# Kernel tuning notes

Hardware: AMD Instinct MI355X
Metric: run time of the kernel (lower is better)

The kernel has to match this reference:

```python
import jax, jax.numpy as jnp
import numpy as np

N, K, E = 262144, 8, 16
DT = 0.02  # config.delta_time


def _mono(x, w1, b1, w2, b2):
    # monotonic_fun with increasing=False: out_linear(exp(-in_linear(x)))
    return jnp.exp(-(x @ w1.T + b1)) @ w2.T + b2


def _isin(a, b):
    # rowwise torch.isin: a [N,P], b [N,Q] -> [N,P] bool
    return (a[:, :, None] == b[:, None, :]).any(-1)


def _angle_clamp(vec, v, ang):
    # torch.cosine_similarity(v, vec, dim=-1).abs() > ang gate (eps=1e-8)
    num = jnp.einsum('nd,nrd->nr', v, vec)
    den = jnp.maximum(jnp.linalg.norm(v, axis=-1)[:, None] * jnp.linalg.norm(vec, axis=-1), 1e-8)
    keep = jnp.abs(num / den) > ang
    return jnp.where(keep[..., None], vec, 0.0)


def _linear_params(key, fan_in, fan_out):
    a = 1.0 / np.sqrt(fan_in)
    k1, k2 = jax.random.split(key)
    # weightConstraint(min_b=0) clamps weights to >= 0 at init
    w = jnp.maximum(jax.random.uniform(k1, (fan_out, fan_in), minval=-a, maxval=a), 0.0)
    b = jax.random.uniform(k2, (fan_out,), minval=-a, maxval=a)
    return w, b


def _mono_params(key):
    k1, k2 = jax.random.split(key)
    w1, b1 = _linear_params(k1, 1, E)
    w2, b2 = _linear_params(k2, E, 1)
    return w1, b1, w2, b2


def setup_inputs() -> dict:
    key = jax.random.key(0)
    ks = jax.random.split(key, 12)
    ego = jax.random.normal(ks[0], (N, 16), dtype=jnp.float32)
    ego = ego.at[:, 0].set(jnp.arange(N, dtype=jnp.float32))
    # surrounding-vehicle id columns 7..14 as small integer ids (floats)
    ego = ego.at[:, 7:15].set(jax.random.randint(ks[1], (N, 8), 0, 21).astype(jnp.float32))
    nei = jax.random.normal(ks[2], (N, K, 16), dtype=jnp.float32)
    nei = nei.at[:, :, 0].set(jax.random.randint(ks[3], (N, K), 1, 21).astype(jnp.float32))
    border = jax.random.uniform(ks[4], (4,), dtype=jnp.float32) * 10.0 + 1.0
    recording_time = jnp.zeros((N, K, 2), dtype=jnp.float32)
    p_dest = jax.random.uniform(ks[5], (2,), dtype=jnp.float32)  # relu(rand(2))
    angle = jax.nn.sigmoid(jax.random.uniform(ks[6], (1,), dtype=jnp.float32))
    d = {'ego': ego, 'nei': nei, 'border': border, 'recording_time': recording_time,
         'p_dest': p_dest, 'angle': angle}
    for name, kk in (('rep', ks[7]), ('att', ks[8]), ('bor', ks[9]), ('del', ks[10])):
        w1, b1, w2, b2 = _mono_params(kk)
        d[name + '_w1'], d[name + '_b1'], d[name + '_w2'], d[name + '_b2'] = w1, b1, w2, b2
    return d


def reference(ego, nei, border, recording_time, p_dest, angle,
              rep_w1, rep_b1, rep_w2, rep_b2,
              att_w1, att_b1, att_w2, att_b2,
              bor_w1, bor_b1, bor_w2, bor_b2,
              del_w1, del_b1, del_w2, del_b2):
    ang = angle[0]
    v = ego[:, 3:5]                                        # ego velocity [N,2]
    speed = jnp.linalg.norm(v, axis=-1)
    desired = jnp.stack([speed, jnp.zeros_like(speed)], axis=1)
    f_dest = ((p_dest[1] * desired - v) / p_dest[0])[:, None, :]   # [N,1,2]

    nei_id = nei[:, :, 0]                                  # [N,K]
    idx = _isin(nei_id, ego[:, 7:15]) & (nei_id != 0)

    # --- recording_time buffer update (vectorized remain/new/pad concat) ---
    buf_id, buf_ct = recording_time[:, :, 0], recording_time[:, :, 1]
    ifin = _isin(buf_id, nei_id)                           # buffer slots still present
    ct2 = buf_ct + ifin.astype(buf_ct.dtype)               # increment their counts
    ifnew = (~_isin(nei_id, buf_id)) & (nei_id != 0)       # brand-new neighbor ids
    cand = jnp.concatenate([jnp.stack([buf_id, ct2], -1),
                            jnp.stack([nei_id, jnp.ones_like(nei_id)], -1)], axis=1)  # [N,2K,2]
    ar = jnp.arange(K)
    BIG = 1 << 20
    keyord = jnp.concatenate([jnp.where(ifin, ar, BIG), jnp.where(ifnew, ar + K, BIG)], axis=1)
    order = jnp.argsort(keyord, axis=1)[:, :K]             # stable: remain order, then new, then pad
    skey = jnp.take_along_axis(keyord, order, axis=1)
    new_buf = jnp.where((skey < BIG)[..., None],
                        jnp.take_along_axis(cand, order[..., None], axis=1), 1.0)  # pad with ones
    count = new_buf[:, :, 1]                               # [N,K]

    # --- neighbor attraction / repulsion ---
    r = jnp.where(idx[..., None], nei[:, :, 1:3] - ego[:, None, 1:3], 0.0)
    rn = jnp.linalg.norm(r, axis=-1)
    rns = jnp.where(idx, rn, 1.0)                          # safe divisor (masked slots zeroed below)
    dirn = r / rns[..., None]
    f_attr = (_mono(count[..., None], del_w1, del_b1, del_w2, del_b2)
              * _mono(rn[..., None], att_w1, att_b1, att_w2, att_b2) * dirn)
    v_nei = nei[:, :, 3:5]
    b = rn + jnp.sum((r + v_nei * DT) ** 2, -1) - jnp.sum((v_nei * DT) ** 2, -1)
    b = jnp.sqrt(jnp.maximum(jnp.where(idx, b, 1.0), 1e-12)) / 2.0
    f_repu = _mono(b[..., None], rep_w1, rep_b1, rep_w2, rep_b2) * dirn
    f_attr = jnp.where(idx[..., None], f_attr, 0.0)
    f_repu = jnp.where(idx[..., None], f_repu, 0.0)

    # --- border repulsion (y-axis only), select_lane = [0, -1] ---
    rb_all = ego[:, 2:3] - border                          # [N,4]
    rb = jnp.stack([rb_all[:, 0], rb_all[:, -1]], axis=1)  # [N,2]
    rbn = jnp.abs(rb)
    f_by = _mono(rbn[..., None], bor_w1, bor_b1, bor_w2, bor_b2) * (rb / rbn)[..., None]
    f_bor = jnp.concatenate([jnp.zeros_like(f_by), f_by], axis=-1)  # [N,2,2]

    f_destination = _angle_clamp(f_dest, v, ang).sum(1)
    f_neighbors = _angle_clamp(f_attr, v, ang).sum(1) + _angle_clamp(f_repu, v, ang).sum(1)
    f_border = _angle_clamp(f_bor, v, ang).sum(1)
    return jnp.stack([f_destination, f_neighbors, f_border], axis=1)  # [N,3,2]
```

## Files before the change

### kernel.cpp

```cpp
#include <hip/hip_runtime.h>
#include <math.h>

#define EN 16

__device__ __forceinline__ float mono_fast(float x,
    const float* __restrict__ w1, const float* __restrict__ b1,
    const float* __restrict__ w2, const float* __restrict__ b2) {
    float acc = 0.0f;
#pragma unroll
    for (int e = 0; e < EN; ++e) {
        float pre = fmaf(x, w1[e], b1[e]);
        acc = fmaf(__expf(-pre), w2[e], acc);
    }
    return acc + b2[0];
}

extern "C" __global__ void __launch_bounds__(256)
sfm_kernel(const float* __restrict__ ego, const float* __restrict__ nei,
           const float* __restrict__ border, const float* __restrict__ rec,
           const float* __restrict__ p_dest, const float* __restrict__ angle,
           const float* __restrict__ rep_w1, const float* __restrict__ rep_b1,
           const float* __restrict__ rep_w2, const float* __restrict__ rep_b2,
           const float* __restrict__ att_w1, const float* __restrict__ att_b1,
           const float* __restrict__ att_w2, const float* __restrict__ att_b2,
           const float* __restrict__ bor_w1, const float* __restrict__ bor_b1,
           const float* __restrict__ bor_w2, const float* __restrict__ bor_b2,
           const float* __restrict__ del_w1, const float* __restrict__ del_b1,
           const float* __restrict__ del_w2, const float* __restrict__ del_b2,
           float* __restrict__ out, int N)
{
    const int gid = blockIdx.x * blockDim.x + threadIdx.x;
    const int n = gid >> 3;
    const int k = gid & 7;
    if (n >= N) return;
    const int lane = threadIdx.x & 63;
    const int gbase = lane & ~7;

    const float ang = angle[0];
    const float p0 = p_dest[0], p1 = p_dest[1];

    const float* er = ego + (size_t)n * 16;
    float4 ea = *(const float4*)(er);
    float4 eb = *(const float4*)(er + 4);
    float4 ec = *(const float4*)(er + 8);
    float4 ed = *(const float4*)(er + 12);
    const float px = ea.y, py = ea.z, vx = ea.w, vy = eb.x;
    const float speed = sqrtf(vx * vx + vy * vy);

    const float* nb = nei + (size_t)n * 128 + (size_t)k * 16;
    float4 na = *(const float4*)nb;
    const float nvyv = nb[4];
    const float nid = na.x;

    float2 rc = *(const float2*)(rec + (size_t)n * 16 + (size_t)k * 2);
    const float bid = rc.x, bct = rc.y;

    bool fin = (bid == nid);
#pragma unroll
    for (int t = 1; t < 8; ++t)
        fin = fin || (bid == __shfl_xor(nid, t));

    unsigned long long bal = __ballot(fin);
    unsigned finM = (unsigned)((bal >> gbase) & 0xFFull);
    int popcFin = __popc(finM);
    int jsel = 0, cbits = 0;
#pragma unroll
    for (int j = 0; j < 8; ++j) {
        int bit = (finM >> j) & 1;
        if (bit && cbits == k) jsel = j;
        cbits += bit;
    }
    float bctj = __shfl(bct, gbase + jsel);
    float cntk = (k < popcFin) ? (bctj + 1.0f) : 1.0f;

    bool match = (nid == eb.w) || (nid == ec.x) || (nid == ec.y) || (nid == ec.z)
              || (nid == ec.w) || (nid == ed.x) || (nid == ed.y) || (nid == ed.z);
    const bool idxk = match && (nid != 0.0f);

    float rx = idxk ? (na.y - px) : 0.0f;
    float ry = idxk ? (na.z - py) : 0.0f;
    float rn = sqrtf(rx * rx + ry * ry);
    float rns = idxk ? rn : 1.0f;
    float dx = rx / rns, dy = ry / rns;

    float att = mono_fast(rn,   att_w1, att_b1, att_w2, att_b2);
    float del = mono_fast(cntk, del_w1, del_b1, del_w2, del_b2);
    float sa = del * att;
    float fax = idxk ? sa * dx : 0.0f;
    float fay = idxk ? sa * dy : 0.0f;

    float nbx = 0.0f, nby = 0.0f;
    {
        float num = vx * fax + vy * fay;
        float fn = sqrtf(fax * fax + fay * fay);
        float den = fmaxf(speed * fn, 1e-8f);
        if (fabsf(num / den) > ang) { nbx += fax; nby += fay; }
    }

    float sxv = na.w * 0.02f, syv = nvyv * 0.02f;
    float ox = rx + sxv, oy = ry + syv;
    float bsum = rn + (ox * ox + oy * oy) - (sxv * sxv + syv * syv);
    float bgate = idxk ? bsum : 1.0f;
    float bb = sqrtf(fmaxf(bgate, 1e-12f)) * 0.5f;
    float rep = mono_fast(bb, rep_w1, rep_b1, rep_w2, rep_b2);
    float frx = idxk ? rep * dx : 0.0f;
    float fry = idxk ? rep * dy : 0.0f;
    {
        float num = vx * frx + vy * fry;
        float fn = sqrtf(frx * frx + fry * fry);
        float den = fmaxf(speed * fn, 1e-8f);
        if (fabsf(num / den) > ang) { nbx += frx; nby += fry; }
    }

    float bsel = (k == 0) ? border[0] : border[3];
    float rb = py - bsel;
    float rbn = fabsf(rb);
    float mb = mono_fast(rbn, bor_w1, bor_b1, bor_w2, bor_b2);
    float fby = mb * (rb / rbn);
    float bory = 0.0f;
    {
        float num = vy * fby;
        float den = fmaxf(speed * fabsf(fby), 1e-8f);
        if ((fabsf(num / den) > ang) && (k < 2)) bory = fby;
    }

#pragma unroll
    for (int m = 1; m < 8; m <<= 1) {
        nbx  += __shfl_xor(nbx,  m);
        nby  += __shfl_xor(nby,  m);
        bory += __shfl_xor(bory, m);
    }

    float fdx = (p1 * speed - vx) / p0;
    float fdy = (0.0f - vy) / p0;
    float fdex = 0.0f, fdey = 0.0f;
    {
        float num = vx * fdx + vy * fdy;
        float fn = sqrtf(fdx * fdx + fdy * fdy);
        float den = fmaxf(speed * fn, 1e-8f);
        if (fabsf(num / den) > ang) { fdex = fdx; fdey = fdy; }
    }

    float wv = (k == 0) ? fdex
             : (k == 1) ? fdey
             : (k == 2) ? nbx
             : (k == 3) ? nby
             : (k == 4) ? 0.0f
             : bory;
    if (k < 6) out[(size_t)n * 6 + k] = wv;
}

extern "C" void kernel_launch(void* const* d_in, const int* in_sizes, int n_in,
                              void* d_out, int out_size, void* d_ws, size_t ws_size,
                              hipStream_t stream) {
    const float* ego    = (const float*)d_in[0];
    const float* nei    = (const float*)d_in[1];
    const float* border = (const float*)d_in[2];
    const float* rec    = (const float*)d_in[3];
    const float* p_dest = (const float*)d_in[4];
    const float* angle  = (const float*)d_in[5];
    const float* rep_w1 = (const float*)d_in[6];
    const float* rep_b1 = (const float*)d_in[7];
    const float* rep_w2 = (const float*)d_in[8];
    const float* rep_b2 = (const float*)d_in[9];
    const float* att_w1 = (const float*)d_in[10];
    const float* att_b1 = (const float*)d_in[11];
    const float* att_w2 = (const float*)d_in[12];
    const float* att_b2 = (const float*)d_in[13];
    const float* bor_w1 = (const float*)d_in[14];
    const float* bor_b1 = (const float*)d_in[15];
    const float* bor_w2 = (const float*)d_in[16];
    const float* bor_b2 = (const float*)d_in[17];
    const float* del_w1 = (const float*)d_in[18];
    const float* del_b1 = (const float*)d_in[19];
    const float* del_w2 = (const float*)d_in[20];
    const float* del_b2 = (const float*)d_in[21];
    float* out = (float*)d_out;

    int N = in_sizes[0] / 16;
    long long threads = (long long)N * 8;
    dim3 grid((unsigned)((threads + 255) / 256));
    sfm_kernel<<<grid, 256, 0, stream>>>(
        ego, nei, border, rec, p_dest, angle,
        rep_w1, rep_b1, rep_w2, rep_b2,
        att_w1, att_b1, att_w2, att_b2,
        bor_w1, bor_b1, bor_w2, bor_b2,
        del_w1, del_b1, del_w2, del_b2,
        out, N);
}
```

Measured before the change: 255.3 us.

## Process all eight neighbors per thread instead of one thread per neighbor

Remaps the kernel from eight lanes per agent to one thread per agent, looping over the eight neighbors in registers. This removes the cross-lane shuffles and ballot, the redundant per-lane ego and destination work, and the six unused border-repulsion evaluations per agent. In exchange, each thread holds many more live registers, which may lower occupancy. Per-thread strided loads of 512-byte neighbor rows may also coalesce worse than the previous layout.

```diff
diff --git a/kernel.cpp b/kernel.cpp
--- a/kernel.cpp
+++ b/kernel.cpp
@@ -29,12 +29,8 @@
            const float* __restrict__ del_w2, const float* __restrict__ del_b2,
            float* __restrict__ out, int N)
 {
-    const int gid = blockIdx.x * blockDim.x + threadIdx.x;
-    const int n = gid >> 3;
-    const int k = gid & 7;
+    const int n = blockIdx.x * blockDim.x + threadIdx.x;
     if (n >= N) return;
-    const int lane = threadIdx.x & 63;
-    const int gbase = lane & ~7;
 
     const float ang = angle[0];
     const float p0 = p_dest[0], p1 = p_dest[1];
@@ -47,88 +43,122 @@
     const float px = ea.y, py = ea.z, vx = ea.w, vy = eb.x;
     const float speed = sqrtf(vx * vx + vy * vy);
 
-    const float* nb = nei + (size_t)n * 128 + (size_t)k * 16;
-    float4 na = *(const float4*)nb;
-    const float nvyv = nb[4];
-    const float nid = na.x;
-
-    float2 rc = *(const float2*)(rec + (size_t)n * 16 + (size_t)k * 2);
-    const float bid = rc.x, bct = rc.y;
-
-    bool fin = (bid == nid);
-#pragma unroll
-    for (int t = 1; t < 8; ++t)
-        fin = fin || (bid == __shfl_xor(nid, t));
-
-    unsigned long long bal = __ballot(fin);
-    unsigned finM = (unsigned)((bal >> gbase) & 0xFFull);
-    int popcFin = __popc(finM);
-    int jsel = 0, cbits = 0;
-#pragma unroll
-    for (int j = 0; j < 8; ++j) {
-        int bit = (finM >> j) & 1;
-        if (bit && cbits == k) jsel = j;
-        cbits += bit;
-    }
-    float bctj = __shfl(bct, gbase + jsel);
-    float cntk = (k < popcFin) ? (bctj + 1.0f) : 1.0f;
-
-    bool match = (nid == eb.w) || (nid == ec.x) || (nid == ec.y) || (nid == ec.z)
-              || (nid == ec.w) || (nid == ed.x) || (nid == ed.y) || (nid == ed.z);
-    const bool idxk = match && (nid != 0.0f);
-
-    float rx = idxk ? (na.y - px) : 0.0f;
-    float ry = idxk ? (na.z - py) : 0.0f;
-    float rn = sqrtf(rx * rx + ry * ry);
-    float rns = idxk ? rn : 1.0f;
-    float dx = rx / rns, dy = ry / rns;
-
-    float att = mono_fast(rn,   att_w1, att_b1, att_w2, att_b2);
-    float del = mono_fast(cntk, del_w1, del_b1, del_w2, del_b2);
-    float sa = del * att;
-    float fax = idxk ? sa * dx : 0.0f;
-    float fay = idxk ? sa * dy : 0.0f;
-
-    float nbx = 0.0f, nby = 0.0f;
+    const float* nb = nei + (size_t)n * 128;
+    float4 na[8]; float nvy[8];
+#pragma unroll
+    for (int k = 0; k < 8; ++k) {
+        na[k]  = *(const float4*)(nb + k * 16);
+        nvy[k] = nb[k * 16 + 4];
+    }
+
+    const float* rr = rec + (size_t)n * 16;
+    float bid[8], bct[8];
+#pragma unroll
+    for (int q = 0; q < 4; ++q) {
+        float4 t = *(const float4*)(rr + q * 4);
+        bid[2*q]   = t.x; bct[2*q]   = t.y;
+        bid[2*q+1] = t.z; bct[2*q+1] = t.w;
+    }
+
+    unsigned finM = 0;
+#pragma unroll
+    for (int k = 0; k < 8; ++k) {
+        bool fin = false;
+#pragma unroll
+        for (int j = 0; j < 8; ++j) fin = fin || (bid[k] == na[j].x);
+        finM |= (fin ? 1u : 0u) << k;
+    }
+    const int popcFin = __popc(finM);
+
+    float cnt[8];
+#pragma unroll
+    for (int k = 0; k < 8; ++k) {
+        int jsel = 0, cbits = 0;
+#pragma unroll
+        for (int j = 0; j < 8; ++j) {
+            int bit = (finM >> j) & 1;
+            if (bit && cbits == k) jsel = j;
+            cbits += bit;
+        }
+        float bj = bct[0];
+#pragma unroll
+        for (int j = 1; j < 8; ++j) bj = (jsel == j) ? bct[j] : bj;
+        cnt[k] = (k < popcFin) ? (bj + 1.0f) : 1.0f;
+    }
+
+    float sx[4] = {0.f, 0.f, 0.f, 0.f}, sy[4] = {0.f, 0.f, 0.f, 0.f};
+#pragma unroll
+    for (int k = 0; k < 8; ++k) {
+        const float nid = na[k].x;
+        bool match = (nid == eb.w) || (nid == ec.x) || (nid == ec.y) || (nid == ec.z)
+                  || (nid == ec.w) || (nid == ed.x) || (nid == ed.y) || (nid == ed.z);
+        const bool idxk = match && (nid != 0.0f);
+
+        float rx = idxk ? (na[k].y - px) : 0.0f;
+        float ry = idxk ? (na[k].z - py) : 0.0f;
+        float rn = sqrtf(rx * rx + ry * ry);
+        float rns = idxk ? rn : 1.0f;
+        float dx = rx / rns, dy = ry / rns;
+
+        float att = mono_fast(rn,     att_w1, att_b1, att_w2, att_b2);
+        float del = mono_fast(cnt[k], del_w1, del_b1, del_w2, del_b2);
+        float sa = del * att;
+        float fax = idxk ? sa * dx : 0.0f;
+        float fay = idxk ? sa * dy : 0.0f;
+
+        float cxk = 0.0f, cyk = 0.0f;
+        {
+            float num = vx * fax + vy * fay;
+            float fn = sqrtf(fax * fax + fay * fay);
+            float den = fmaxf(speed * fn, 1e-8f);
+            if (fabsf(num / den) > ang) { cxk += fax; cyk += fay; }
+        }
+
+        float sxv = na[k].w * 0.02f, syv = nvy[k] * 0.02f;
+        float ox = rx + sxv, oy = ry + syv;
+        float bsum = rn + (ox * ox + oy * oy) - (sxv * sxv + syv * syv);
+        float bgate = idxk ? bsum : 1.0f;
+        float bb = sqrtf(fmaxf(bgate, 1e-12f)) * 0.5f;
+        float rep = mono_fast(bb, rep_w1, rep_b1, rep_w2, rep_b2);
+        float frx = idxk ? rep * dx : 0.0f;
+        float fry = idxk ? rep * dy : 0.0f;
+        {
+            float num = vx * frx + vy * fry;
+            float fn = sqrtf(frx * frx + fry * fry);
+            float den = fmaxf(speed * fn, 1e-8f);
+            if (fabsf(num / den) > ang) { cxk += frx; cyk += fry; }
+        }
+
+        sx[k >> 1] += cxk;
+        sy[k >> 1] += cyk;
+    }
+    const float nbx = (sx[0] + sx[1]) + (sx[2] + sx[3]);
+    const float nby = (sy[0] + sy[1]) + (sy[2] + sy[3]);
+
+    float bory;
     {
-        float num = vx * fax + vy * fay;
-        float fn = sqrtf(fax * fax + fay * fay);
-        float den = fmaxf(speed * fn, 1e-8f);
-        if (fabsf(num / den) > ang) { nbx += fax; nby += fay; }
-    }
-
-    float sxv = na.w * 0.02f, syv = nvyv * 0.02f;
-    float ox = rx + sxv, oy = ry + syv;
-    float bsum = rn + (ox * ox + oy * oy) - (sxv * sxv + syv * syv);
-    float bgate = idxk ? bsum : 1.0f;
-    float bb = sqrtf(fmaxf(bgate, 1e-12f)) * 0.5f;
-    float rep = mono_fast(bb, rep_w1, rep_b1, rep_w2, rep_b2);
-    float frx = idxk ? rep * dx : 0.0f;
-    float fry = idxk ? rep * dy : 0.0f;
-    {
-        float num = vx * frx + vy * fry;
-        float fn = sqrtf(frx * frx + fry * fry);
-        float den = fmaxf(speed * fn, 1e-8f);
-        if (fabsf(num / den) > ang) { nbx += frx; nby += fry; }
-    }
-
-    float bsel = (k == 0) ? border[0] : border[3];
-    float rb = py - bsel;
-    float rbn = fabsf(rb);
-    float mb = mono_fast(rbn, bor_w1, bor_b1, bor_w2, bor_b2);
-    float fby = mb * (rb / rbn);
-    float bory = 0.0f;
-    {
-        float num = vy * fby;
-        float den = fmaxf(speed * fabsf(fby), 1e-8f);
-        if ((fabsf(num / den) > ang) && (k < 2)) bory = fby;
-    }
-
-#pragma unroll
-    for (int m = 1; m < 8; m <<= 1) {
-        nbx  += __shfl_xor(nbx,  m);
-        nby  += __shfl_xor(nby,  m);
-        bory += __shfl_xor(bory, m);
+        float b0v = border[0], b3v = border[3];
+
+        float rb0 = py - b0v, rbn0 = fabsf(rb0);
+        float mb0 = mono_fast(rbn0, bor_w1, bor_b1, bor_w2, bor_b2);
+        float fby0 = mb0 * (rb0 / rbn0);
+        float g0 = 0.0f;
+        {
+            float num = vy * fby0;
+            float den = fmaxf(speed * fabsf(fby0), 1e-8f);
+            if (fabsf(num / den) > ang) g0 = fby0;
+        }
+
+        float rb1 = py - b3v, rbn1 = fabsf(rb1);
+        float mb1 = mono_fast(rbn1, bor_w1, bor_b1, bor_w2, bor_b2);
+        float fby1 = mb1 * (rb1 / rbn1);
+        float g1 = 0.0f;
+        {
+            float num = vy * fby1;
+            float den = fmaxf(speed * fabsf(fby1), 1e-8f);
+            if (fabsf(num / den) > ang) g1 = fby1;
+        }
+        bory = g0 + g1;
     }
 
     float fdx = (p1 * speed - vx) / p0;
@@ -141,13 +171,10 @@
         if (fabsf(num / den) > ang) { fdex = fdx; fdey = fdy; }
     }
 
-    float wv = (k == 0) ? fdex
-             : (k == 1) ? fdey
-             : (k == 2) ? nbx
-             : (k == 3) ? nby
-             : (k == 4) ? 0.0f
-             : bory;
-    if (k < 6) out[(size_t)n * 6 + k] = wv;
+    float2* o = (float2*)(out + (size_t)n * 6);
+    o[0] = make_float2(fdex, fdey);
+    o[1] = make_float2(nbx, nby);
+    o[2] = make_float2(0.0f, bory);
 }
 
 extern "C" void kernel_launch(void* const* d_in, const int* in_sizes, int n_in,
@@ -178,8 +205,7 @@
     float* out = (float*)d_out;
 
     int N = in_sizes[0] / 16;
-    long long threads = (long long)N * 8;
-    dim3 grid((unsigned)((threads + 255) / 256));
+    dim3 grid((unsigned)((N + 255) / 256));
     sfm_kernel<<<grid, 256, 0, stream>>>(
         ego, nei, border, rec, p_dest, angle,
         rep_w1, rep_b1, rep_w2, rep_b2,
```

After: 272.5 us. 1.07x slower.

## Process two neighbors per thread with four lanes per agent

Applied to the files above, without the earlier changes.

Remaps the kernel so each agent uses four lanes instead of eight, with each lane handling two neighbors. The recording-time lookup is rebuilt from two ballots and interleaved bitmasks, and outputs are written as float2. This halves the redundant per-lane ego loads, border evaluations, destination math and shuffle-reduction steps. The cost is more registers and serial work per thread, and less thread-level parallelism for hiding memory latency.

```diff
diff --git a/kernel.cpp b/kernel.cpp
--- a/kernel.cpp
+++ b/kernel.cpp
@@ -13,6 +13,60 @@
         acc = fmaf(__expf(-pre), w2[e], acc);
     }
     return acc + b2[0];
+}
+
+__device__ __forceinline__ void do_neighbor(
+    float4 na, float nvy, float cntk,
+    float px, float py, float vx, float vy, float speed, float ang,
+    float m0, float m1, float m2, float m3,
+    float m4, float m5, float m6, float m7,
+    const float* __restrict__ rep_w1, const float* __restrict__ rep_b1,
+    const float* __restrict__ rep_w2, const float* __restrict__ rep_b2,
+    const float* __restrict__ att_w1, const float* __restrict__ att_b1,
+    const float* __restrict__ att_w2, const float* __restrict__ att_b2,
+    const float* __restrict__ del_w1, const float* __restrict__ del_b1,
+    const float* __restrict__ del_w2, const float* __restrict__ del_b2,
+    float& cxk, float& cyk)
+{
+    const float nid = na.x;
+    bool match = (nid == m0) || (nid == m1) || (nid == m2) || (nid == m3)
+              || (nid == m4) || (nid == m5) || (nid == m6) || (nid == m7);
+    const bool idxk = match && (nid != 0.0f);
+
+    float rx = idxk ? (na.y - px) : 0.0f;
+    float ry = idxk ? (na.z - py) : 0.0f;
+    float rn = sqrtf(rx * rx + ry * ry);
+    float rns = idxk ? rn : 1.0f;
+    float dx = rx / rns, dy = ry / rns;
+
+    float att = mono_fast(rn,   att_w1, att_b1, att_w2, att_b2);
+    float del = mono_fast(cntk, del_w1, del_b1, del_w2, del_b2);
+    float sa = del * att;
+    float fax = idxk ? sa * dx : 0.0f;
+    float fay = idxk ? sa * dy : 0.0f;
+
+    cxk = 0.0f; cyk = 0.0f;
+    {
+        float num = vx * fax + vy * fay;
+        float fn = sqrtf(fax * fax + fay * fay);
+        float den = fmaxf(speed * fn, 1e-8f);
+        if (fabsf(num / den) > ang) { cxk += fax; cyk += fay; }
+    }
+
+    float sxv = na.w * 0.02f, syv = nvy * 0.02f;
+    float ox = rx + sxv, oy = ry + syv;
+    float bsum = rn + (ox * ox + oy * oy) - (sxv * sxv + syv * syv);
+    float bgate = idxk ? bsum : 1.0f;
+    float bb = sqrtf(fmaxf(bgate, 1e-12f)) * 0.5f;
+    float rep = mono_fast(bb, rep_w1, rep_b1, rep_w2, rep_b2);
+    float frx = idxk ? rep * dx : 0.0f;
+    float fry = idxk ? rep * dy : 0.0f;
+    {
+        float num = vx * frx + vy * fry;
+        float fn = sqrtf(frx * frx + fry * fry);
+        float den = fmaxf(speed * fn, 1e-8f);
+        if (fabsf(num / den) > ang) { cxk += frx; cyk += fry; }
+    }
 }
 
 extern "C" __global__ void __launch_bounds__(256)
@@ -30,11 +84,11 @@
            float* __restrict__ out, int N)
 {
     const int gid = blockIdx.x * blockDim.x + threadIdx.x;
-    const int n = gid >> 3;
-    const int k = gid & 7;
+    const int n = gid >> 2;
+    const int s = gid & 3;
     if (n >= N) return;
     const int lane = threadIdx.x & 63;
-    const int gbase = lane & ~7;
+    const int gbase = lane & ~3;
 
     const float ang = angle[0];
     const float p0 = p_dest[0], p1 = p_dest[1];
@@ -46,90 +100,86 @@
     float4 ed = *(const float4*)(er + 12);
     const float px = ea.y, py = ea.z, vx = ea.w, vy = eb.x;
     const float speed = sqrtf(vx * vx + vy * vy);
-
-    const float* nb = nei + (size_t)n * 128 + (size_t)k * 16;
-    float4 na = *(const float4*)nb;
-    const float nvyv = nb[4];
-    const float nid = na.x;
-
-    float2 rc = *(const float2*)(rec + (size_t)n * 16 + (size_t)k * 2);
-    const float bid = rc.x, bct = rc.y;
-
-    bool fin = (bid == nid);
-#pragma unroll
-    for (int t = 1; t < 8; ++t)
-        fin = fin || (bid == __shfl_xor(nid, t));
-
-    unsigned long long bal = __ballot(fin);
-    unsigned finM = (unsigned)((bal >> gbase) & 0xFFull);
-    int popcFin = __popc(finM);
-    int jsel = 0, cbits = 0;
-#pragma unroll
-    for (int j = 0; j < 8; ++j) {
-        int bit = (finM >> j) & 1;
-        if (bit && cbits == k) jsel = j;
-        cbits += bit;
-    }
-    float bctj = __shfl(bct, gbase + jsel);
-    float cntk = (k < popcFin) ? (bctj + 1.0f) : 1.0f;
-
-    bool match = (nid == eb.w) || (nid == ec.x) || (nid == ec.y) || (nid == ec.z)
-              || (nid == ec.w) || (nid == ed.x) || (nid == ed.y) || (nid == ed.z);
-    const bool idxk = match && (nid != 0.0f);
-
-    float rx = idxk ? (na.y - px) : 0.0f;
-    float ry = idxk ? (na.z - py) : 0.0f;
-    float rn = sqrtf(rx * rx + ry * ry);
-    float rns = idxk ? rn : 1.0f;
-    float dx = rx / rns, dy = ry / rns;
-
-    float att = mono_fast(rn,   att_w1, att_b1, att_w2, att_b2);
-    float del = mono_fast(cntk, del_w1, del_b1, del_w2, del_b2);
-    float sa = del * att;
-    float fax = idxk ? sa * dx : 0.0f;
-    float fay = idxk ? sa * dy : 0.0f;
-
-    float nbx = 0.0f, nby = 0.0f;
-    {
-        float num = vx * fax + vy * fay;
-        float fn = sqrtf(fax * fax + fay * fay);
-        float den = fmaxf(speed * fn, 1e-8f);
-        if (fabsf(num / den) > ang) { nbx += fax; nby += fay; }
-    }
-
-    float sxv = na.w * 0.02f, syv = nvyv * 0.02f;
-    float ox = rx + sxv, oy = ry + syv;
-    float bsum = rn + (ox * ox + oy * oy) - (sxv * sxv + syv * syv);
-    float bgate = idxk ? bsum : 1.0f;
-    float bb = sqrtf(fmaxf(bgate, 1e-12f)) * 0.5f;
-    float rep = mono_fast(bb, rep_w1, rep_b1, rep_w2, rep_b2);
-    float frx = idxk ? rep * dx : 0.0f;
-    float fry = idxk ? rep * dy : 0.0f;
-    {
-        float num = vx * frx + vy * fry;
-        float fn = sqrtf(frx * frx + fry * fry);
-        float den = fmaxf(speed * fn, 1e-8f);
-        if (fabsf(num / den) > ang) { nbx += frx; nby += fry; }
-    }
-
-    float bsel = (k == 0) ? border[0] : border[3];
-    float rb = py - bsel;
-    float rbn = fabsf(rb);
-    float mb = mono_fast(rbn, bor_w1, bor_b1, bor_w2, bor_b2);
-    float fby = mb * (rb / rbn);
-    float bory = 0.0f;
-    {
+    const float m0 = eb.w, m1 = ec.x, m2 = ec.y, m3 = ec.z;
+    const float m4 = ec.w, m5 = ed.x, m6 = ed.y, m7 = ed.z;
+
+    const int k0 = 2 * s, k1 = 2 * s + 1;
+    const float* nb = nei + (size_t)n * 128;
+    float4 na0 = *(const float4*)(nb + k0 * 16);
+    float  nv0 = nb[k0 * 16 + 4];
+    float4 na1 = *(const float4*)(nb + k1 * 16);
+    float  nv1 = nb[k1 * 16 + 4];
+
+    float4 rcv = *(const float4*)(rec + (size_t)n * 16 + s * 4);
+    const float bidA = rcv.x, bctA = rcv.y;
+    const float bidB = rcv.z, bctB = rcv.w;
+
+    const float g0 = na0.x, g1 = na1.x;
+    const float x1a = __shfl_xor(g0, 1), x1b = __shfl_xor(g1, 1);
+    const float x2a = __shfl_xor(g0, 2), x2b = __shfl_xor(g1, 2);
+    const float x3a = __shfl_xor(g0, 3), x3b = __shfl_xor(g1, 3);
+
+    bool finA = (bidA == g0) || (bidA == g1) || (bidA == x1a) || (bidA == x1b)
+             || (bidA == x2a) || (bidA == x2b) || (bidA == x3a) || (bidA == x3b);
+    bool finB = (bidB == g0) || (bidB == g1) || (bidB == x1a) || (bidB == x1b)
+             || (bidB == x2a) || (bidB == x2b) || (bidB == x3a) || (bidB == x3b);
+
+    unsigned long long balA = __ballot(finA);
+    unsigned long long balB = __ballot(finB);
+    unsigned mA = (unsigned)((balA >> gbase) & 0xFull);
+    unsigned mB = (unsigned)((balB >> gbase) & 0xFull);
+    unsigned finM = 0;
+#pragma unroll
+    for (int l = 0; l < 4; ++l)
+        finM |= (((mA >> l) & 1u) << (2 * l)) | (((mB >> l) & 1u) << (2 * l + 1));
+    const int popcFin = __popc(finM);
+
+    float cntv[2];
+#pragma unroll
+    for (int t = 0; t < 2; ++t) {
+        const int k = 2 * s + t;
+        int jsel = 0, cbits = 0;
+#pragma unroll
+        for (int j = 0; j < 8; ++j) {
+            int bit = (finM >> j) & 1;
+            if (bit && cbits == k) jsel = j;
+            cbits += bit;
+        }
+        int owner = gbase + (jsel >> 1);
+        float lo = __shfl(bctA, owner);
+        float hi = __shfl(bctB, owner);
+        float bj = (jsel & 1) ? hi : lo;
+        cntv[t] = (k < popcFin) ? (bj + 1.0f) : 1.0f;
+    }
+
+    float cx0, cy0, cx1, cy1;
+    do_neighbor(na0, nv0, cntv[0], px, py, vx, vy, speed, ang,
+                m0, m1, m2, m3, m4, m5, m6, m7,
+                rep_w1, rep_b1, rep_w2, rep_b2,
+                att_w1, att_b1, att_w2, att_b2,
+                del_w1, del_b1, del_w2, del_b2, cx0, cy0);
+    do_neighbor(na1, nv1, cntv[1], px, py, vx, vy, speed, ang,
+                m0, m1, m2, m3, m4, m5, m6, m7,
+                rep_w1, rep_b1, rep_w2, rep_b2,
+                att_w1, att_b1, att_w2, att_b2,
+                del_w1, del_b1, del_w2, del_b2, cx1, cy1);
+    float pxs = cx0 + cx1;
+    float pys = cy0 + cy1;
+
+    float gb = 0.0f;
+    {
+        float bsel = (s == 1) ? border[3] : border[0];
+        float rb = py - bsel;
+        float rbn = fabsf(rb);
+        float mb = mono_fast(rbn, bor_w1, bor_b1, bor_w2, bor_b2);
+        float fby = mb * (rb / rbn);
         float num = vy * fby;
         float den = fmaxf(speed * fabsf(fby), 1e-8f);
-        if ((fabsf(num / den) > ang) && (k < 2)) bory = fby;
-    }
-
-#pragma unroll
-    for (int m = 1; m < 8; m <<= 1) {
-        nbx  += __shfl_xor(nbx,  m);
-        nby  += __shfl_xor(nby,  m);
-        bory += __shfl_xor(bory, m);
-    }
+        if ((fabsf(num / den) > ang) && (s < 2)) gb = fby;
+    }
+
+    pxs += __shfl_xor(pxs, 1);  pys += __shfl_xor(pys, 1);  gb += __shfl_xor(gb, 1);
+    pxs += __shfl_xor(pxs, 2);  pys += __shfl_xor(pys, 2);  gb += __shfl_xor(gb, 2);
 
     float fdx = (p1 * speed - vx) / p0;
     float fdy = (0.0f - vy) / p0;
@@ -141,13 +191,10 @@
         if (fabsf(num / den) > ang) { fdex = fdx; fdey = fdy; }
     }
 
-    float wv = (k == 0) ? fdex
-             : (k == 1) ? fdey
-             : (k == 2) ? nbx
-             : (k == 3) ? nby
-             : (k == 4) ? 0.0f
-             : bory;
-    if (k < 6) out[(size_t)n * 6 + k] = wv;
+    float2 wv = (s == 0) ? make_float2(fdex, fdey)
+              : (s == 1) ? make_float2(pxs, pys)
+              :            make_float2(0.0f, gb);
+    if (s < 3) *(float2*)(out + (size_t)n * 6 + 2 * s) = wv;
 }
 
 extern "C" void kernel_launch(void* const* d_in, const int* in_sizes, int n_in,
@@ -178,7 +225,7 @@
     float* out = (float*)d_out;
 
     int N = in_sizes[0] / 16;
-    long long threads = (long long)N * 8;
+    long long threads = (long long)N * 4;
     dim3 grid((unsigned)((threads + 255) / 256));
     sfm_kernel<<<grid, 256, 0, stream>>>(
         ego, nei, border, rec, p_dest, angle,
```

Measured after the change: 254.3 us. About the same (-0.4%).
